# Performance work log

Hardware: AMD Instinct MI355X
Metric: run time of the kernel (lower is better)

Reference implementation:

```python
import jax, jax.numpy as jnp
import numpy as np

DIM = 1024
N_HEADS = 8
N_KV_HEADS = 8
Q_C = 128
Q_NOPE = 96
Q_ROPE = 32
KV_C = 128
K_NOPE = 64
K_ROPE = 64
V_HD = 256
EPS = 1e-8
ROPE_THETA = 10000.0


def rms_norm(x, w, eps=EPS):
    return w * x * jax.lax.rsqrt(jnp.mean(x * x, axis=-1, keepdims=True) + eps)


def apply_rope(x, position_ids, head_dim):
    # x: [B, H, S, hd], interleaved even/odd rotation (matches torch module)
    inv_freq = 1.0 / (ROPE_THETA ** (jnp.arange(0, head_dim, 2, dtype=jnp.float32) / head_dim))
    ang = position_ids.astype(jnp.float32)[:, None, :, None] * inv_freq  # [B,1,S,hd/2]
    cos, sin = jnp.cos(ang), jnp.sin(ang)
    xe, xo = x[..., ::2], x[..., 1::2]
    rot = jnp.stack((xe * cos - xo * sin, xe * sin + xo * cos), axis=-1)
    return rot.reshape(x.shape)


def setup_inputs() -> dict:
    key = jax.random.key(0)
    ks = jax.random.split(key, 12)
    B, S = 2, 2048
    s = 0.02
    return {
        "x": jax.random.normal(ks[0], (B, S, DIM), jnp.float32),
        "position_ids": jnp.broadcast_to(jnp.arange(S, dtype=jnp.int32), (B, S)),
        "w_dq_w": jax.random.normal(ks[1], (DIM, Q_C), jnp.float32) * s,
        "w_dq_b": jnp.zeros((Q_C,), jnp.float32),
        "q_norm_w": jnp.ones((Q_C,), jnp.float32),
        "w_uq_qr_w": jax.random.normal(ks[2], (Q_C, N_HEADS * (Q_NOPE + Q_ROPE)), jnp.float32) * s,
        "w_uq_qr_b": jnp.zeros((N_HEADS * (Q_NOPE + Q_ROPE),), jnp.float32),
        "w_dkv_kr_w": jax.random.normal(ks[3], (DIM, KV_C + K_ROPE), jnp.float32) * s,
        "w_dkv_kr_b": jnp.zeros((KV_C + K_ROPE,), jnp.float32),
        "kv_norm_w": jnp.ones((KV_C,), jnp.float32),
        "w_uk_uv_w": jax.random.normal(ks[4], (KV_C, N_KV_HEADS * (K_NOPE + V_HD)), jnp.float32) * s,
        "w_uk_uv_b": jnp.zeros((N_KV_HEADS * (K_NOPE + V_HD),), jnp.float32),
        "w_o_w": jax.random.normal(ks[5], (N_HEADS * V_HD, DIM), jnp.float32) * s,
        "w_o_b": jnp.zeros((DIM,), jnp.float32),
    }


def reference(x, position_ids, w_dq_w, w_dq_b, q_norm_w, w_uq_qr_w, w_uq_qr_b,
              w_dkv_kr_w, w_dkv_kr_b, kv_norm_w, w_uk_uv_w, w_uk_uv_b, w_o_w, w_o_b):
    B, S, _ = x.shape
    # --- Q path: compress -> norm -> up-project, split nope/rope ---
    cq = rms_norm(x @ w_dq_w + w_dq_b, q_norm_w)                     # [B,S,Qc]
    q = cq @ w_uq_qr_w + w_uq_qr_b                                   # [B,S,H*(96+32)]
    q_nope, q_rope = jnp.split(q, [N_HEADS * Q_NOPE], axis=-1)
    q_nope = q_nope.reshape(B, S, N_HEADS, Q_NOPE).transpose(0, 2, 1, 3)
    q_rope = q_rope.reshape(B, S, N_HEADS, Q_ROPE).transpose(0, 2, 1, 3)
    q_rope = apply_rope(q_rope, position_ids, Q_ROPE)
    q_states = jnp.concatenate((q_nope, q_rope), axis=-1)            # [B,H,S,128]
    # --- KV path: compress + shared rope key ---
    ckv_kr = x @ w_dkv_kr_w + w_dkv_kr_b
    ckv, k_rope = jnp.split(ckv_kr, [KV_C], axis=-1)
    ckv = rms_norm(ckv, kv_norm_w)                                   # [B,S,KVc]
    k_rope = apply_rope(k_rope[:, None, :, :], position_ids, K_ROPE) # [B,1,S,64]
    kv = ckv @ w_uk_uv_w + w_uk_uv_b                                 # [B,S,KVh*(64+256)]
    k_nope, v = jnp.split(kv, [N_KV_HEADS * K_NOPE], axis=-1)
    k_nope = k_nope.reshape(B, S, N_KV_HEADS, K_NOPE).transpose(0, 2, 1, 3)
    k_rope = jnp.broadcast_to(k_rope, (B, N_KV_HEADS, S, K_ROPE))
    k_states = jnp.concatenate((k_nope, k_rope), axis=-1)            # [B,KVh,S,128]
    v_states = v.reshape(B, S, N_KV_HEADS, V_HD).transpose(0, 2, 1, 3)
    # gqa_factor = n_heads // n_kv_heads = 1 -> repeat is a no-op
    # --- SDPA (no mask), scale = 1/sqrt(q head dim) ---
    scale = 1.0 / jnp.sqrt(jnp.float32(Q_NOPE + Q_ROPE))
    scores = jnp.einsum("bhqd,bhkd->bhqk", q_states, k_states) * scale
    probs = jax.nn.softmax(scores, axis=-1)
    attn = jnp.einsum("bhqk,bhkd->bhqd", probs, v_states)            # [B,H,S,256]
    attn = attn.transpose(0, 2, 1, 3).reshape(B, S, N_HEADS * V_HD)
    return attn @ w_o_w + w_o_b
```

## Files before the change

### kernel.cpp

```cpp
#include <hip/hip_runtime.h>
#include <hip/hip_bf16.h>
#include <stdint.h>

typedef unsigned short u16;
typedef short short8 __attribute__((ext_vector_type(8)));
typedef float floatx4 __attribute__((ext_vector_type(4)));

#define S_LEN 2048
#define NB 2
#define NH 8
#define R_TOK (NB * S_LEN)

#define L2_THETA 13.287712379549449f
#define QSCALE (0.08838834764831845f * 1.4426950408889634f)

__device__ inline u16 f2bf(float f) {
  union { float f; uint32_t u; } x; x.f = f;
  uint32_t r = (x.u + 0x7fffu + ((x.u >> 16) & 1u)) >> 16;
  return (u16)r;
}
__device__ inline float bf2f(u16 h) {
  union { uint32_t u; float f; } x; x.u = ((uint32_t)h) << 16;
  return x.f;
}
__device__ inline floatx4 mfma16(short8 a, short8 b, floatx4 c) {
  return __builtin_amdgcn_mfma_f32_16x16x32_bf16(a, b, c, 0, 0, 0);
}
__device__ inline uint32_t pkbf(float a, float b) {
  union { __hip_bfloat162 h; uint32_t u; } c;
  c.h = __float22bfloat162_rn(make_float2(a, b));
  return c.u;
}
__device__ __forceinline__ void cp16(const void* g, const void* l) {
  __builtin_amdgcn_global_load_lds(
      (const __attribute__((address_space(1))) uint32_t*)(uintptr_t)g,
      (__attribute__((address_space(3))) uint32_t*)(uintptr_t)l, 16, 0, 0);
}

__global__ __launch_bounds__(256) void k_prep(
    const float* __restrict__ x, u16* __restrict__ xbf,
    const float* __restrict__ wdq, const float* __restrict__ wdkv, u16* __restrict__ waT,
    const float* __restrict__ wuq, u16* __restrict__ wQT,
    const float* __restrict__ wukv, u16* __restrict__ wKVT,
    const float* __restrict__ wo, u16* __restrict__ wOT,
    const float* __restrict__ bdq, const float* __restrict__ bdkv,
    float* __restrict__ biasA) {
  __shared__ u16 tile[32][33];
  const int s = blockIdx.x, tid = threadIdx.x;
  const int tx = tid & 31, ty = tid >> 5;
  if (s < 4096) {
    int i = s * 256 + tid;
    float4 v = ((const float4*)x)[i];
    ushort4 o;
    o.x = f2bf(v.x); o.y = f2bf(v.y); o.z = f2bf(v.z); o.w = f2bf(v.w);
    ((ushort4*)xbf)[i] = o;
  } else if (s < 4416) {
    int t = s - 4096, bx = t % 10, by = t / 10;
    int c0 = bx * 32, r0 = by * 32;
#pragma unroll
    for (int i = 0; i < 4; ++i) {
      int r = r0 + ty + i * 8, c = c0 + tx;
      float v = (c < 128) ? wdq[(size_t)r * 128 + c] : wdkv[(size_t)r * 192 + (c - 128)];
      tile[ty + i * 8][tx] = f2bf(v);
    }
    __syncthreads();
#pragma unroll
    for (int i = 0; i < 4; ++i)
      waT[(size_t)(c0 + ty + i * 8) * 1024 + r0 + tx] = tile[tx][ty + i * 8];
  } else {
    const float* in; u16* out; int R, C, bx, by;
    if (s < 4544) { int t = s - 4416; in = wuq; out = wQT; R = 128; C = 1024; bx = t & 31; by = t >> 5; }
    else if (s < 4864) { int t = s - 4544; in = wukv; out = wKVT; R = 128; C = 2560; bx = t % 80; by = t / 80; }
    else if (s < 6912) { int t = s - 4864; in = wo; out = wOT; R = 2048; C = 1024; bx = t & 31; by = t >> 5; }
    else {
      if (tid < 320) biasA[tid] = (tid < 128) ? bdq[tid] : bdkv[tid - 128];
      return;
    }
    int c0 = bx * 32, r0 = by * 32;
#pragma unroll
    for (int i = 0; i < 4; ++i)
      tile[ty + i * 8][tx] = f2bf(in[(size_t)(r0 + ty + i * 8) * C + c0 + tx]);
    __syncthreads();
#pragma unroll
    for (int i = 0; i < 4; ++i)
      out[(size_t)(c0 + ty + i * 8) * R + r0 + tx] = tile[tx][ty + i * 8];
  }
}

template <int OUT_BF>
__global__ __launch_bounds__(256) void k_gemm_bt(const u16* __restrict__ A,
                                                 const u16* __restrict__ BT,
                                                 const float* __restrict__ bias,
                                                 void* __restrict__ Cout,
                                                 int M, int N, int K) {
  __shared__ __align__(16) u16 Alds[2][128 * 32];
  __shared__ __align__(16) u16 Blds[2][128 * 32];
  const int tid = threadIdx.x;
  const int wave = tid >> 6, lane = tid & 63;
  const int lane15 = lane & 15, quad = lane >> 4;
  const int m0 = blockIdx.y * 128, n0 = blockIdx.x * 128;
  const int mw = (wave & 1) * 64, nw = (wave >> 1) * 64;

  floatx4 acc[4][4];
#pragma unroll
  for (int a = 0; a < 4; ++a)
#pragma unroll
    for (int b = 0; b < 4; ++b) acc[a][b] = (floatx4){0.f, 0.f, 0.f, 0.f};

  const int srow = wave * 32 + (lane >> 2);
  const int scol = (lane & 3) * 8;

  auto stage = [&](int k0, int buf) {
    const u16* ga = A + (size_t)(m0 + srow) * K + k0 + scol;
    cp16(ga, Alds[buf] + srow * 32 + scol);
    cp16(ga + (size_t)16 * K, Alds[buf] + (srow + 16) * 32 + scol);
    const u16* gb = BT + (size_t)(n0 + srow) * K + k0 + scol;
    cp16(gb, Blds[buf] + srow * 32 + scol);
    cp16(gb + (size_t)16 * K, Blds[buf] + (srow + 16) * 32 + scol);
  };

  stage(0, 0);
  int cur = 0;
  for (int k0 = 0; k0 < K; k0 += 32) {
    __syncthreads();
    if (k0 + 32 < K) stage(k0 + 32, cur ^ 1);
    short8 af[4], bf[4];
#pragma unroll
    for (int im = 0; im < 4; ++im)
      af[im] = *(const short8*)&Alds[cur][(mw + im * 16 + lane15) * 32 + quad * 8];
#pragma unroll
    for (int in = 0; in < 4; ++in)
      bf[in] = *(const short8*)&Blds[cur][(nw + in * 16 + lane15) * 32 + quad * 8];
#pragma unroll
    for (int im = 0; im < 4; ++im)
#pragma unroll
      for (int in = 0; in < 4; ++in) acc[im][in] = mfma16(af[im], bf[in], acc[im][in]);
    cur ^= 1;
  }

#pragma unroll
  for (int im = 0; im < 4; ++im)
#pragma unroll
    for (int in = 0; in < 4; ++in)
#pragma unroll
      for (int r = 0; r < 4; ++r) {
        int row = m0 + mw + im * 16 + quad * 4 + r;
        int col = n0 + nw + in * 16 + lane15;
        if (col < N) {
          float v = acc[im][in][r] + bias[col];
          if (OUT_BF)
            ((u16*)Cout)[(size_t)row * N + col] = f2bf(v);
          else
            ((float*)Cout)[(size_t)row * N + col] = v;
        }
      }
}

__global__ __launch_bounds__(256) void k_gemm_q(const u16* __restrict__ A,
                                                const u16* __restrict__ BT,
                                                const float* __restrict__ bias,
                                                const float* __restrict__ qtab,
                                                u16* __restrict__ qstates) {
  const int K = 128;
  __shared__ __align__(16) u16 Alds[2][128 * 32];
  __shared__ __align__(16) u16 Blds[2][128 * 32];
  const int tid = threadIdx.x;
  const int wave = tid >> 6, lane = tid & 63;
  const int lane15 = lane & 15, quad = lane >> 4;
  const int m0 = blockIdx.x * 128, n0 = blockIdx.y * 128;
  const int mw = (wave & 1) * 64, nw = (wave >> 1) * 64;

  floatx4 acc[4][4];
#pragma unroll
  for (int a = 0; a < 4; ++a)
#pragma unroll
    for (int b = 0; b < 4; ++b) acc[a][b] = (floatx4){0.f, 0.f, 0.f, 0.f};

  const int srow = wave * 32 + (lane >> 2);
  const int scol = (lane & 3) * 8;
  auto stage = [&](int k0, int buf) {
    const u16* ga = A + (size_t)(m0 + srow) * K + k0 + scol;
    cp16(ga, Alds[buf] + srow * 32 + scol);
    cp16(ga + (size_t)16 * K, Alds[buf] + (srow + 16) * 32 + scol);
    const u16* gb = BT + (size_t)(n0 + srow) * K + k0 + scol;
    cp16(gb, Blds[buf] + srow * 32 + scol);
    cp16(gb + (size_t)16 * K, Blds[buf] + (srow + 16) * 32 + scol);
  };

  stage(0, 0);
  int cur = 0;
  for (int k0 = 0; k0 < K; k0 += 32) {
    __syncthreads();
    if (k0 + 32 < K) stage(k0 + 32, cur ^ 1);
    short8 af[4], bf[4];
#pragma unroll
    for (int im = 0; im < 4; ++im)
      af[im] = *(const short8*)&Alds[cur][(mw + im * 16 + lane15) * 32 + quad * 8];
#pragma unroll
    for (int in = 0; in < 4; ++in)
      bf[in] = *(const short8*)&Blds[cur][(nw + in * 16 + lane15) * 32 + quad * 8];
#pragma unroll
    for (int im = 0; im < 4; ++im)
#pragma unroll
      for (int in = 0; in < 4; ++in) acc[im][in] = mfma16(af[im], bf[in], acc[im][in]);
    cur ^= 1;
  }

  const bool ropeblk = (n0 >= 768);
#pragma unroll
  for (int in = 0; in < 4; ++in) {
    const int col = n0 + nw + in * 16 + lane15;
#pragma unroll
    for (int im = 0; im < 4; ++im) {
      if (!ropeblk) {
        const int h = col / 96, d = col - h * 96;
#pragma unroll
        for (int r = 0; r < 4; ++r) {
          int row = m0 + mw + im * 16 + quad * 4 + r;
          int b = row >> 11, s = row & (S_LEN - 1);
          float v = acc[im][in][r] + bias[col];
          qstates[((size_t)(b * NH + h) * S_LEN + s) * 128 + d] = f2bf(v * QSCALE);
        }
      } else {
        const int j = (col - 768) & 31, h = (col - 768) >> 5, pr = j >> 1;
#pragma unroll
        for (int r = 0; r < 4; ++r) {
          int row = m0 + mw + im * 16 + quad * 4 + r;
          int b = row >> 11, s = row & (S_LEN - 1);
          float v = acc[im][in][r] + bias[col];
          float vp = __shfl_xor(v, 1);
          float xe = (lane & 1) ? vp : v;
          float xo = (lane & 1) ? v : vp;
          float2 cs = *(const float2*)&qtab[((size_t)row * 16 + pr) * 2];
          float val = (j & 1) ? (xe * cs.y + xo * cs.x) : (xe * cs.x - xo * cs.y);
          qstates[((size_t)(b * NH + h) * S_LEN + s) * 128 + 96 + j] = f2bf(val * QSCALE);
        }
      }
    }
  }
}

__global__ __launch_bounds__(256) void k_gemm_kv(const u16* __restrict__ A,
                                                 const u16* __restrict__ BT,
                                                 const float* __restrict__ bias,
                                                 u16* __restrict__ kvb,
                                                 u16* __restrict__ vT) {
  const int K = 128, N = 2560;
  __shared__ __align__(16) u16 Alds[2][128 * 32];
  __shared__ __align__(16) u16 Blds[2][128 * 32];
  __shared__ __align__(16) u16 eplds[64 * 136];
  const int tid = threadIdx.x;
  const int wave = tid >> 6, lane = tid & 63;
  const int lane15 = lane & 15, quad = lane >> 4;
  const int m0 = blockIdx.y * 128, n0 = blockIdx.x * 128;
  const int mw = (wave & 1) * 64, nw = (wave >> 1) * 64;

  floatx4 acc[4][4];
#pragma unroll
  for (int a = 0; a < 4; ++a)
#pragma unroll
    for (int b = 0; b < 4; ++b) acc[a][b] = (floatx4){0.f, 0.f, 0.f, 0.f};

  const int srow = wave * 32 + (lane >> 2);
  const int scol = (lane & 3) * 8;
  auto stage = [&](int k0, int buf) {
    const u16* ga = A + (size_t)(m0 + srow) * K + k0 + scol;
    cp16(ga, Alds[buf] + srow * 32 + scol);
    cp16(ga + (size_t)16 * K, Alds[buf] + (srow + 16) * 32 + scol);
    const u16* gb = BT + (size_t)(n0 + srow) * K + k0 + scol;
    cp16(gb, Blds[buf] + srow * 32 + scol);
    cp16(gb + (size_t)16 * K, Blds[buf] + (srow + 16) * 32 + scol);
  };

  stage(0, 0);
  int cur = 0;
  for (int k0 = 0; k0 < K; k0 += 32) {
    __syncthreads();
    if (k0 + 32 < K) stage(k0 + 32, cur ^ 1);
    short8 af[4], bf[4];
#pragma unroll
    for (int im = 0; im < 4; ++im)
      af[im] = *(const short8*)&Alds[cur][(mw + im * 16 + lane15) * 32 + quad * 8];
#pragma unroll
    for (int in = 0; in < 4; ++in)
      bf[in] = *(const short8*)&Blds[cur][(nw + in * 16 + lane15) * 32 + quad * 8];
#pragma unroll
    for (int im = 0; im < 4; ++im)
#pragma unroll
      for (int in = 0; in < 4; ++in) acc[im][in] = mfma16(af[im], bf[in], acc[im][in]);
    cur ^= 1;
  }

  if (n0 < 512) {
#pragma unroll
    for (int im = 0; im < 4; ++im)
#pragma unroll
      for (int in = 0; in < 4; ++in)
#pragma unroll
        for (int r = 0; r < 4; ++r) {
          int row = m0 + mw + im * 16 + quad * 4 + r;
          int col = n0 + nw + in * 16 + lane15;
          kvb[(size_t)row * N + col] = f2bf(acc[im][in][r] + bias[col]);
        }
  } else {
    const int sbase = m0 & (S_LEN - 1), bq = m0 >> 11;
#pragma unroll
    for (int hh = 0; hh < 2; ++hh) {
#pragma unroll
      for (int im = 0; im < 4; ++im) {
        const int rrel = mw + im * 16 + quad * 4;
        const int bb = (rrel & 63) >> 2;
        const int a = (bb & 8) | (((bb >> 1) & 1) << 2) | ((bb & 1) << 1) | ((bb >> 2) & 1);
        const int prel = (rrel >> 6) * 64 + a * 4;
#pragma unroll
        for (int ii = 0; ii < 2; ++ii) {
          const int in = hh * 2 + ii;
          const int nl = nw + in * 16 + lane15;
          const int slot = (nl & 31) | ((nl & 64) >> 1);
          const float bv = bias[n0 + nl];
          ushort4 o;
          o.x = f2bf(acc[im][in][0] + bv);
          o.y = f2bf(acc[im][in][1] + bv);
          o.z = f2bf(acc[im][in][2] + bv);
          o.w = f2bf(acc[im][in][3] + bv);
          *(ushort4*)&eplds[slot * 136 + prel] = o;
        }
      }
      __syncthreads();
#pragma unroll
      for (int i = 0; i < 4; ++i) {
        int idx = i * 256 + tid;
        int slot = idx >> 4, c8 = (idx & 15) * 8;
        int nl = (slot & 31) + hh * 32 + ((slot & 32) << 1);
        int c2 = n0 + nl - 512;
        int hv = c2 >> 8, nn = c2 & 255;
        short8 v = *(const short8*)&eplds[slot * 136 + c8];
        *(short8*)&vT[((size_t)((bq * NH + hv) * 256 + nn)) * 2048 + sbase + c8] = v;
      }
      if (hh == 0) __syncthreads();
    }
  }
}

__global__ void k_stagea(const float* __restrict__ t0, const float* __restrict__ qnw,
                         const float* __restrict__ kvnw, const int* __restrict__ pos_ids,
                         u16* __restrict__ cq, u16* __restrict__ ckv,
                         u16* __restrict__ krope, float* __restrict__ qtab) {
  int r = blockIdx.x, tid = threadIdx.x;
  const float* row = t0 + (size_t)r * 320;
  float a = row[tid];
  float b = row[128 + tid];
  float sa = a * a, sb = b * b;
#pragma unroll
  for (int d = 1; d < 64; d <<= 1) {
    sa += __shfl_xor(sa, d);
    sb += __shfl_xor(sb, d);
  }
  __shared__ float red[4];
  if ((tid & 63) == 0) { red[(tid >> 6) * 2] = sa; red[(tid >> 6) * 2 + 1] = sb; }
  __syncthreads();
  sa = red[0] + red[2];
  sb = red[1] + red[3];
  float ra = rsqrtf(sa * (1.0f / 128.0f) + 1e-8f);
  float rb = rsqrtf(sb * (1.0f / 128.0f) + 1e-8f);
  cq[(size_t)r * 128 + tid] = f2bf(qnw[tid] * a * ra);
  ckv[(size_t)r * 128 + tid] = f2bf(kvnw[tid] * b * rb);
  if (tid < 32) {
    float xe = row[256 + 2 * tid], xo = row[256 + 2 * tid + 1];
    float p = (float)pos_ids[r];
    float freq = exp2f(-(2.0f * tid / 64.0f) * L2_THETA);
    float ang = p * freq;
    float c = cosf(ang), s = sinf(ang);
    krope[(size_t)r * 64 + 2 * tid] = f2bf(xe * c - xo * s);
    krope[(size_t)r * 64 + 2 * tid + 1] = f2bf(xe * s + xo * c);
  } else if (tid < 48) {
    int pr = tid - 32;
    float p = (float)pos_ids[r];
    float freq = exp2f(-(2.0f * pr / 32.0f) * L2_THETA);
    float ang = p * freq;
    qtab[((size_t)r * 16 + pr) * 2] = cosf(ang);
    qtab[((size_t)r * 16 + pr) * 2 + 1] = sinf(ang);
  }
}

__global__ __launch_bounds__(512) void k_attn(const u16* __restrict__ qstates,
                                              const u16* __restrict__ kv,
                                              const u16* __restrict__ krope,
                                              const u16* __restrict__ vT,
                                              u16* __restrict__ attn_out) {
  const int pair = blockIdx.x;
  const int qblk = blockIdx.y;
  const int b = pair >> 3, h = pair & 7;
  const int tid = threadIdx.x;
  const int wave = tid >> 6, lane = tid & 63;
  const int lane15 = lane & 15, quad = lane >> 4;
  const int w4 = wave & 3, half = wave >> 2;

  __shared__ __align__(16) u16 Klds[2][64 * 128];
  __shared__ __align__(16) u16 Vlds[2][256 * 64];

  const int qrow0 = qblk * 128 + wave * 16;
  short8 qfrag[4];
  {
    const u16* qb = qstates + ((size_t)(b * NH + h) * S_LEN + qrow0 + lane15) * 128 + quad * 8;
#pragma unroll
    for (int c = 0; c < 4; ++c) qfrag[c] = *(const short8*)(qb + c * 32);
  }

  floatx4 o_acc[16];
#pragma unroll
  for (int g = 0; g < 16; ++g) o_acc[g] = (floatx4){0.f, 0.f, 0.f, 0.f};
  float m_i = -1e30f;
  float l_i = 0.f;

  const int kbase = (quad * 16 + lane15) * 8;
  int vo0[4], vo1[4];
#pragma unroll
  for (int ph = 0; ph < 4; ++ph) {
    int n = ph * 16 + lane15;
    int sw = (n ^ (n >> 3)) & 7;
    vo0[ph] = n * 64 + ((quad ^ sw) & 7) * 8;
    vo1[ph] = n * 64 + (((quad | 4) ^ sw) & 7) * 8;
  }

  const u16* kp[2];
  int kstr[2];
  int kdst[2];
#pragma unroll
  for (int j = 0; j < 2; ++j) {
    int u = half * 8 + j * 4 + quad;
    const u16* base;
    int str;
    if (u < 8) { base = kv + h * 64 + u * 8; str = 2560; }
    else { base = krope + (u - 8) * 8; str = 64; }
    kp[j] = base + (size_t)(b * S_LEN + w4 * 16 + lane15) * str;
    kstr[j] = str;
    kdst[j] = (w4 * 256 + (half * 2 + j) * 64 + lane) * 8;
  }
  const int vn6 = tid >> 3, vsl = tid & 7;
  const u16* vp[4];
#pragma unroll
  for (int oi = 0; oi < 4; ++oi) {
    int n = oi * 64 + vn6;
    int u = vsl ^ ((n ^ (n >> 3)) & 7);
    vp[oi] = vT + ((size_t)pair * 256 + n) * 2048 + u * 8;
  }

  auto issueK = [&](int buf) {
#pragma unroll
    for (int j = 0; j < 2; ++j) {
      cp16(kp[j], &Klds[buf][kdst[j]]);
      kp[j] += (size_t)64 * kstr[j];
    }
  };
  auto issueV = [&](int buf) {
#pragma unroll
    for (int oi = 0; oi < 4; ++oi) {
      cp16(vp[oi], &Vlds[buf][(oi * 512 + tid) * 8]);
      vp[oi] += 64;
    }
  };

  issueK(0);
  issueV(0);
  asm volatile("s_waitcnt vmcnt(0)" ::: "memory");
  __builtin_amdgcn_sched_barrier(0);
  __builtin_amdgcn_s_barrier();

  int cur = 0;
  for (int ch = 0; ch < S_LEN / 64; ++ch) {
    if (ch + 1 < S_LEN / 64) {
      issueK(cur ^ 1);
      issueV(cur ^ 1);
    }

    floatx4 st[4];
#pragma unroll
    for (int t = 0; t < 4; ++t) st[t] = (floatx4){0.f, 0.f, 0.f, 0.f};
    __builtin_amdgcn_s_setprio(1);
#pragma unroll
    for (int c = 0; c < 4; ++c) {
      short8 qf = qfrag[c];
#pragma unroll
      for (int t = 0; t < 4; ++t) {
        short8 kf = *(const short8*)&Klds[cur][kbase + (t * 16 + c * 4) * 128];
        st[t] = mfma16(kf, qf, st[t]);
      }
    }
    __builtin_amdgcn_s_setprio(0);

    float mloc = st[0][0];
#pragma unroll
    for (int t = 0; t < 4; ++t)
#pragma unroll
      for (int r = 0; r < 4; ++r) mloc = fmaxf(mloc, st[t][r]);
    mloc = fmaxf(mloc, __shfl_xor(mloc, 16));
    mloc = fmaxf(mloc, __shfl_xor(mloc, 32));

    const bool resc = __any(mloc > m_i + 8.0f);
    const float mref = resc ? fmaxf(m_i, mloc) : m_i;

    float rs = 0.f;
    union { short8 s; uint4 u; } a01, a23;
    {
      float p0, p1, p2, p3;
      p0 = exp2f(st[0][0] - mref); p1 = exp2f(st[0][1] - mref);
      p2 = exp2f(st[0][2] - mref); p3 = exp2f(st[0][3] - mref);
      rs += (p0 + p1) + (p2 + p3);
      a01.u.x = pkbf(p0, p1); a01.u.y = pkbf(p2, p3);
      p0 = exp2f(st[1][0] - mref); p1 = exp2f(st[1][1] - mref);
      p2 = exp2f(st[1][2] - mref); p3 = exp2f(st[1][3] - mref);
      rs += (p0 + p1) + (p2 + p3);
      a01.u.z = pkbf(p0, p1); a01.u.w = pkbf(p2, p3);
      p0 = exp2f(st[2][0] - mref); p1 = exp2f(st[2][1] - mref);
      p2 = exp2f(st[2][2] - mref); p3 = exp2f(st[2][3] - mref);
      rs += (p0 + p1) + (p2 + p3);
      a23.u.x = pkbf(p0, p1); a23.u.y = pkbf(p2, p3);
      p0 = exp2f(st[3][0] - mref); p1 = exp2f(st[3][1] - mref);
      p2 = exp2f(st[3][2] - mref); p3 = exp2f(st[3][3] - mref);
      rs += (p0 + p1) + (p2 + p3);
      a23.u.z = pkbf(p0, p1); a23.u.w = pkbf(p2, p3);
    }

    if (resc) {
      float alpha = exp2f(m_i - mref);
      m_i = mref;
      l_i = l_i * alpha + rs;
      float al[4];
#pragma unroll
      for (int r = 0; r < 4; ++r) al[r] = __shfl(alpha, quad * 4 + r, 16);
#pragma unroll
      for (int g = 0; g < 16; ++g) {
        o_acc[g][0] *= al[0]; o_acc[g][1] *= al[1];
        o_acc[g][2] *= al[2]; o_acc[g][3] *= al[3];
      }
    } else {
      l_i += rs;
    }

    __builtin_amdgcn_s_setprio(1);
#pragma unroll
    for (int g = 0; g < 16; ++g) {
      short8 b01 = *(const short8*)&Vlds[cur][vo0[g & 3] + (g >> 2) * 4096];
      short8 b23 = *(const short8*)&Vlds[cur][vo1[g & 3] + (g >> 2) * 4096];
      floatx4 o = o_acc[g];
      o = mfma16(a01.s, b01, o);
      o = mfma16(a23.s, b23, o);
      o_acc[g] = o;
    }
    __builtin_amdgcn_s_setprio(0);

    asm volatile("s_waitcnt vmcnt(0)" ::: "memory");
    __builtin_amdgcn_sched_barrier(0);
    __builtin_amdgcn_s_barrier();
    cur ^= 1;
  }

  float lsum = l_i;
  lsum += __shfl_xor(lsum, 16);
  lsum += __shfl_xor(lsum, 32);
  float rl = 1.0f / lsum;
  float linv[4];
#pragma unroll
  for (int r = 0; r < 4; ++r) linv[r] = __shfl(rl, quad * 4 + r, 16);
#pragma unroll
  for (int g = 0; g < 16; ++g) {
#pragma unroll
    for (int r = 0; r < 4; ++r) {
      int row = qrow0 + quad * 4 + r;
      int col = h * 256 + g * 16 + lane15;
      attn_out[((size_t)b * S_LEN + row) * 2048 + col] = f2bf(o_acc[g][r] * linv[r]);
    }
  }
}

extern "C" void kernel_launch(void* const* d_in, const int* in_sizes, int n_in,
                              void* d_out, int out_size, void* d_ws, size_t ws_size,
                              hipStream_t stream) {
  const float* x = (const float*)d_in[0];
  const int* pos = (const int*)d_in[1];
  const float* wdq = (const float*)d_in[2];
  const float* bdq = (const float*)d_in[3];
  const float* qnw = (const float*)d_in[4];
  const float* wuq = (const float*)d_in[5];
  const float* buq = (const float*)d_in[6];
  const float* wdkv = (const float*)d_in[7];
  const float* bdkv = (const float*)d_in[8];
  const float* kvnw = (const float*)d_in[9];
  const float* wukv = (const float*)d_in[10];
  const float* bukv = (const float*)d_in[11];
  const float* wo = (const float*)d_in[12];
  const float* bo = (const float*)d_in[13];
  float* out = (float*)d_out;

  char* ws = (char*)d_ws;
  size_t off = 0;
  auto alloc = [&](size_t bytes) {
    char* p = ws + off;
    off += (bytes + 255) & ~(size_t)255;
    return p;
  };
  u16* xbf = (u16*)alloc((size_t)R_TOK * 1024 * 2);
  float* t0 = (float*)alloc((size_t)R_TOK * 320 * 4);
  u16* qout = (u16*)alloc((size_t)R_TOK * 1024 * 2);
  u16* vT = (u16*)d_ws;
  u16* waT = (u16*)alloc((size_t)384 * 1024 * 2);
  float* biasA = (float*)alloc(320 * 4);
  u16* wQT = (u16*)alloc((size_t)1024 * 128 * 2);
  u16* wKVT = (u16*)alloc((size_t)2560 * 128 * 2);
  u16* wOT = (u16*)alloc((size_t)1024 * 2048 * 2);
  u16* cq = (u16*)alloc((size_t)R_TOK * 128 * 2);
  u16* ckv = (u16*)alloc((size_t)R_TOK * 128 * 2);
  u16* krope = (u16*)alloc((size_t)R_TOK * 64 * 2);
  u16* qst = (u16*)alloc((size_t)R_TOK * 1024 * 2);
  u16* kvb = (u16*)alloc((size_t)R_TOK * 2560 * 2);
  u16* attnb = (u16*)alloc((size_t)R_TOK * 2048 * 2);
  float* qtab = (float*)alloc((size_t)R_TOK * 16 * 2 * 4);
  (void)ws_size; (void)n_in; (void)in_sizes; (void)out_size; (void)qout;

  k_prep<<<6913, 256, 0, stream>>>(x, xbf, wdq, wdkv, waT, wuq, wQT, wukv, wKVT, wo, wOT,
                                   bdq, bdkv, biasA);

  k_gemm_bt<0><<<dim3(3, 32), 256, 0, stream>>>(xbf, waT, biasA, t0, R_TOK, 320, 1024);
  k_stagea<<<R_TOK, 128, 0, stream>>>(t0, qnw, kvnw, pos, cq, ckv, krope, qtab);
  k_gemm_q<<<dim3(32, 8), 256, 0, stream>>>(cq, wQT, buq, qtab, qst);
  k_gemm_kv<<<dim3(20, 32), 256, 0, stream>>>(ckv, wKVT, bukv, kvb, vT);
  k_attn<<<dim3(16, 16), 512, 0, stream>>>(qst, kvb, krope, vT, attnb);
  k_gemm_bt<0><<<dim3(8, 32), 256, 0, stream>>>(attnb, wOT, bo, out, R_TOK, 1024, 2048);
}
```

Before: 259.0 us.

## Process two 16-row query subtiles per wave in attention, halving block threads

```diff
diff --git a/kernel.cpp b/kernel.cpp
--- a/kernel.cpp
+++ b/kernel.cpp
@@ -383,35 +383,38 @@
   }
 }
 
-__global__ __launch_bounds__(512) void k_attn(const u16* __restrict__ qstates,
-                                              const u16* __restrict__ kv,
-                                              const u16* __restrict__ krope,
-                                              const u16* __restrict__ vT,
-                                              u16* __restrict__ attn_out) {
+__global__ __launch_bounds__(256, 1) void k_attn(const u16* __restrict__ qstates,
+                                                 const u16* __restrict__ kv,
+                                                 const u16* __restrict__ krope,
+                                                 const u16* __restrict__ vT,
+                                                 u16* __restrict__ attn_out) {
   const int pair = blockIdx.x;
   const int qblk = blockIdx.y;
   const int b = pair >> 3, h = pair & 7;
   const int tid = threadIdx.x;
   const int wave = tid >> 6, lane = tid & 63;
   const int lane15 = lane & 15, quad = lane >> 4;
-  const int w4 = wave & 3, half = wave >> 2;
 
   __shared__ __align__(16) u16 Klds[2][64 * 128];
   __shared__ __align__(16) u16 Vlds[2][256 * 64];
 
-  const int qrow0 = qblk * 128 + wave * 16;
-  short8 qfrag[4];
-  {
-    const u16* qb = qstates + ((size_t)(b * NH + h) * S_LEN + qrow0 + lane15) * 128 + quad * 8;
-#pragma unroll
-    for (int c = 0; c < 4; ++c) qfrag[c] = *(const short8*)(qb + c * 32);
-  }
-
-  floatx4 o_acc[16];
-#pragma unroll
-  for (int g = 0; g < 16; ++g) o_acc[g] = (floatx4){0.f, 0.f, 0.f, 0.f};
-  float m_i = -1e30f;
-  float l_i = 0.f;
+  const int qrow0 = qblk * 128 + wave * 32;
+  short8 qfrag[2][4];
+#pragma unroll
+  for (int s = 0; s < 2; ++s) {
+    const u16* qb =
+        qstates + ((size_t)(b * NH + h) * S_LEN + qrow0 + s * 16 + lane15) * 128 + quad * 8;
+#pragma unroll
+    for (int c = 0; c < 4; ++c) qfrag[s][c] = *(const short8*)(qb + c * 32);
+  }
+
+  floatx4 o_acc[2][16];
+#pragma unroll
+  for (int s = 0; s < 2; ++s)
+#pragma unroll
+    for (int g = 0; g < 16; ++g) o_acc[s][g] = (floatx4){0.f, 0.f, 0.f, 0.f};
+  float m_i[2] = {-1e30f, -1e30f};
+  float l_i[2] = {0.f, 0.f};
 
   const int kbase = (quad * 16 + lane15) * 8;
   int vo0[4], vo1[4];
@@ -423,40 +426,37 @@
     vo1[ph] = n * 64 + (((quad | 4) ^ sw) & 7) * 8;
   }
 
-  const u16* kp[2];
-  int kstr[2];
-  int kdst[2];
-#pragma unroll
-  for (int j = 0; j < 2; ++j) {
-    int u = half * 8 + j * 4 + quad;
+  const u16* kp[4];
+  int kstr[4];
+#pragma unroll
+  for (int j = 0; j < 4; ++j) {
+    int u = 4 * j + quad;
     const u16* base;
     int str;
     if (u < 8) { base = kv + h * 64 + u * 8; str = 2560; }
     else { base = krope + (u - 8) * 8; str = 64; }
-    kp[j] = base + (size_t)(b * S_LEN + w4 * 16 + lane15) * str;
+    kp[j] = base + (size_t)(b * S_LEN + wave * 16 + lane15) * str;
     kstr[j] = str;
-    kdst[j] = (w4 * 256 + (half * 2 + j) * 64 + lane) * 8;
-  }
-  const int vn6 = tid >> 3, vsl = tid & 7;
-  const u16* vp[4];
-#pragma unroll
-  for (int oi = 0; oi < 4; ++oi) {
-    int n = oi * 64 + vn6;
+  }
+  auto issueK = [&](int buf) {
+#pragma unroll
+    for (int j = 0; j < 4; ++j) {
+      cp16(kp[j], &Klds[buf][((wave * 16 + 4 * j) * 16 + lane) * 8]);
+      kp[j] += (size_t)64 * kstr[j];
+    }
+  };
+  const int vn5 = tid >> 3, vsl = tid & 7;
+  const u16* vp[8];
+#pragma unroll
+  for (int oi = 0; oi < 8; ++oi) {
+    int n = oi * 32 + vn5;
     int u = vsl ^ ((n ^ (n >> 3)) & 7);
     vp[oi] = vT + ((size_t)pair * 256 + n) * 2048 + u * 8;
   }
-
-  auto issueK = [&](int buf) {
-#pragma unroll
-    for (int j = 0; j < 2; ++j) {
-      cp16(kp[j], &Klds[buf][kdst[j]]);
-      kp[j] += (size_t)64 * kstr[j];
-    }
-  };
   auto issueV = [&](int buf) {
 #pragma unroll
-    for (int oi = 0; oi < 4; ++oi) {
-      cp16(vp[oi], &Vlds[buf][(oi * 512 + tid) * 8]);
+    for (int oi = 0; oi < 8; ++oi) {
+      cp16(vp[oi], &Vlds[buf][(oi * 256 + tid) * 8]);
       vp[oi] += 64;
     }
   };
@@ -474,68 +474,73 @@
       issueV(cur ^ 1);
     }
 
-    floatx4 st[4];
-#pragma unroll
-    for (int t = 0; t < 4; ++t) st[t] = (floatx4){0.f, 0.f, 0.f, 0.f};
+    floatx4 st[2][4];
+#pragma unroll
+    for (int s = 0; s < 2; ++s)
+#pragma unroll
+      for (int t = 0; t < 4; ++t) st[s][t] = (floatx4){0.f, 0.f, 0.f, 0.f};
     __builtin_amdgcn_s_setprio(1);
 #pragma unroll
     for (int c = 0; c < 4; ++c) {
-      short8 qf = qfrag[c];
 #pragma unroll
       for (int t = 0; t < 4; ++t) {
         short8 kf = *(const short8*)&Klds[cur][kbase + (t * 16 + c * 4) * 128];
-        st[t] = mfma16(kf, qf, st[t]);
+        st[0][t] = mfma16(kf, qfrag[0][c], st[0][t]);
+        st[1][t] = mfma16(kf, qfrag[1][c], st[1][t]);
       }
     }
     __builtin_amdgcn_s_setprio(0);
 
-    float mloc = st[0][0];
-#pragma unroll
-    for (int t = 0; t < 4; ++t)
-#pragma unroll
-      for (int r = 0; r < 4; ++r) mloc = fmaxf(mloc, st[t][r]);
-    mloc = fmaxf(mloc, __shfl_xor(mloc, 16));
-    mloc = fmaxf(mloc, __shfl_xor(mloc, 32));
-
-    const bool resc = __any(mloc > m_i + 8.0f);
-    const float mref = resc ? fmaxf(m_i, mloc) : m_i;
-
-    float rs = 0.f;
-    union { short8 s; uint4 u; } a01, a23;
-    {
-      float p0, p1, p2, p3;
-      p0 = exp2f(st[0][0] - mref); p1 = exp2f(st[0][1] - mref);
-      p2 = exp2f(st[0][2] - mref); p3 = exp2f(st[0][3] - mref);
-      rs += (p0 + p1) + (p2 + p3);
-      a01.u.x = pkbf(p0, p1); a01.u.y = pkbf(p2, p3);
-      p0 = exp2f(st[1][0] - mref); p1 = exp2f(st[1][1] - mref);
-      p2 = exp2f(st[1][2] - mref); p3 = exp2f(st[1][3] - mref);
-      rs += (p0 + p1) + (p2 + p3);
-      a01.u.z = pkbf(p0, p1); a01.u.w = pkbf(p2, p3);
-      p0 = exp2f(st[2][0] - mref); p1 = exp2f(st[2][1] - mref);
-      p2 = exp2f(st[2][2] - mref); p3 = exp2f(st[2][3] - mref);
-      rs += (p0 + p1) + (p2 + p3);
-      a23.u.x = pkbf(p0, p1); a23.u.y = pkbf(p2, p3);
-      p0 = exp2f(st[3][0] - mref); p1 = exp2f(st[3][1] - mref);
-      p2 = exp2f(st[3][2] - mref); p3 = exp2f(st[3][3] - mref);
-      rs += (p0 + p1) + (p2 + p3);
-      a23.u.z = pkbf(p0, p1); a23.u.w = pkbf(p2, p3);
-    }
-
-    if (resc) {
-      float alpha = exp2f(m_i - mref);
-      m_i = mref;
-      l_i = l_i * alpha + rs;
-      float al[4];
-#pragma unroll
-      for (int r = 0; r < 4; ++r) al[r] = __shfl(alpha, quad * 4 + r, 16);
-#pragma unroll
-      for (int g = 0; g < 16; ++g) {
-        o_acc[g][0] *= al[0]; o_acc[g][1] *= al[1];
-        o_acc[g][2] *= al[2]; o_acc[g][3] *= al[3];
-      }
-    } else {
-      l_i += rs;
+    union { short8 s; uint4 u; } a01[2], a23[2];
+#pragma unroll
+    for (int s = 0; s < 2; ++s) {
+      float mloc = st[s][0][0];
+#pragma unroll
+      for (int t = 0; t < 4; ++t)
+#pragma unroll
+        for (int r = 0; r < 4; ++r) mloc = fmaxf(mloc, st[s][t][r]);
+      mloc = fmaxf(mloc, __shfl_xor(mloc, 16));
+      mloc = fmaxf(mloc, __shfl_xor(mloc, 32));
+
+      const bool resc = __any(mloc > m_i[s] + 8.0f);
+      const float mref = resc ? fmaxf(m_i[s], mloc) : m_i[s];
+
+      float rs = 0.f;
+      {
+        float p0, p1, p2, p3;
+        p0 = exp2f(st[s][0][0] - mref); p1 = exp2f(st[s][0][1] - mref);
+        p2 = exp2f(st[s][0][2] - mref); p3 = exp2f(st[s][0][3] - mref);
+        rs += (p0 + p1) + (p2 + p3);
+        a01[s].u.x = pkbf(p0, p1); a01[s].u.y = pkbf(p2, p3);
+        p0 = exp2f(st[s][1][0] - mref); p1 = exp2f(st[s][1][1] - mref);
+        p2 = exp2f(st[s][1][2] - mref); p3 = exp2f(st[s][1][3] - mref);
+        rs += (p0 + p1) + (p2 + p3);
+        a01[s].u.z = pkbf(p0, p1); a01[s].u.w = pkbf(p2, p3);
+        p0 = exp2f(st[s][2][0] - mref); p1 = exp2f(st[s][2][1] - mref);
+        p2 = exp2f(st[s][2][2] - mref); p3 = exp2f(st[s][2][3] - mref);
+        rs += (p0 + p1) + (p2 + p3);
+        a23[s].u.x = pkbf(p0, p1); a23[s].u.y = pkbf(p2, p3);
+        p0 = exp2f(st[s][3][0] - mref); p1 = exp2f(st[s][3][1] - mref);
+        p2 = exp2f(st[s][3][2] - mref); p3 = exp2f(st[s][3][3] - mref);
+        rs += (p0 + p1) + (p2 + p3);
+        a23[s].u.z = pkbf(p0, p1); a23[s].u.w = pkbf(p2, p3);
+      }
+
+      if (resc) {
+        float alpha = exp2f(m_i[s] - mref);
+        m_i[s] = mref;
+        l_i[s] = l_i[s] * alpha + rs;
+        float al[4];
+#pragma unroll
+        for (int r = 0; r < 4; ++r) al[r] = __shfl(alpha, quad * 4 + r, 16);
+#pragma unroll
+        for (int g = 0; g < 16; ++g) {
+          o_acc[s][g][0] *= al[0]; o_acc[s][g][1] *= al[1];
+          o_acc[s][g][2] *= al[2]; o_acc[s][g][3] *= al[3];
+        }
+      } else {
+        l_i[s] += rs;
+      }
     }
 
     __builtin_amdgcn_s_setprio(1);
@@ -543,10 +548,10 @@
     for (int g = 0; g < 16; ++g) {
       short8 b01 = *(const short8*)&Vlds[cur][vo0[g & 3] + (g >> 2) * 4096];
       short8 b23 = *(const short8*)&Vlds[cur][vo1[g & 3] + (g >> 2) * 4096];
-      floatx4 o = o_acc[g];
-      o = mfma16(a01.s, b01, o);
-      o = mfma16(a23.s, b23, o);
-      o_acc[g] = o;
+      o_acc[0][g] = mfma16(a01[0].s, b01, o_acc[0][g]);
+      o_acc[1][g] = mfma16(a01[1].s, b01, o_acc[1][g]);
+      o_acc[0][g] = mfma16(a23[0].s, b23, o_acc[0][g]);
+      o_acc[1][g] = mfma16(a23[1].s, b23, o_acc[1][g]);
     }
     __builtin_amdgcn_s_setprio(0);
 
@@ -556,20 +561,23 @@
     cur ^= 1;
   }
 
-  float lsum = l_i;
-  lsum += __shfl_xor(lsum, 16);
-  lsum += __shfl_xor(lsum, 32);
-  float rl = 1.0f / lsum;
-  float linv[4];
-#pragma unroll
-  for (int r = 0; r < 4; ++r) linv[r] = __shfl(rl, quad * 4 + r, 16);
-#pragma unroll
-  for (int g = 0; g < 16; ++g) {
-#pragma unroll
-    for (int r = 0; r < 4; ++r) {
-      int row = qrow0 + quad * 4 + r;
-      int col = h * 256 + g * 16 + lane15;
-      attn_out[((size_t)b * S_LEN + row) * 2048 + col] = f2bf(o_acc[g][r] * linv[r]);
+#pragma unroll
+  for (int s = 0; s < 2; ++s) {
+    float lsum = l_i[s];
+    lsum += __shfl_xor(lsum, 16);
+    lsum += __shfl_xor(lsum, 32);
+    float rl = 1.0f / lsum;
+    float linv[4];
+#pragma unroll
+    for (int r = 0; r < 4; ++r) linv[r] = __shfl(rl, quad * 4 + r, 16);
+#pragma unroll
+    for (int g = 0; g < 16; ++g) {
+#pragma unroll
+      for (int r = 0; r < 4; ++r) {
+        int row = qrow0 + s * 16 + quad * 4 + r;
+        int col = h * 256 + g * 16 + lane15;
+        attn_out[((size_t)b * S_LEN + row) * 2048 + col] = f2bf(o_acc[s][g][r] * linv[r]);
+      }
     }
   }
 }
@@ -625,6 +633,6 @@
   k_stagea<<<R_TOK, 128, 0, stream>>>(t0, qnw, kvnw, pos, cq, ckv, krope, qtab);
   k_gemm_q<<<dim3(32, 8), 256, 0, stream>>>(cq, wQT, buq, qtab, qst);
   k_gemm_kv<<<dim3(20, 32), 256, 0, stream>>>(ckv, wKVT, bukv, kvb, vT);
-  k_attn<<<dim3(16, 16), 512, 0, stream>>>(qst, kvb, krope, vT, attnb);
+  k_attn<<<dim3(16, 16), 256, 0, stream>>>(qst, kvb, krope, vT, attnb);
   k_gemm_bt<0><<<dim3(8, 32), 256, 0, stream>>>(attnb, wOT, bo, out, R_TOK, 1024, 2048);
 }
```

Measured after the change: 274.7 us. 1.06x slower.
